# Kernel optimization log

Hardware: AMD Instinct MI355X
Metric: run time of the kernel (lower is better)

Reference implementation:

```python
import jax, jax.numpy as jnp
import numpy as np


def setup_inputs() -> dict:
    key = jax.random.key(0)
    k1, k2, k3, k4 = jax.random.split(key, 4)
    bs, n, f_in, f_out, n_head = 4, 2048, 64, 64, 8
    h = jax.random.normal(k1, (bs, n, f_in), dtype=jnp.float32)
    adj = jnp.ones((bs, n, n), dtype=bool)  # accepted by forward but unused
    # xavier-uniform-like init scales
    w = jax.random.uniform(k2, (n_head, f_in, f_out), dtype=jnp.float32,
                           minval=-1.0, maxval=1.0) * np.sqrt(6.0 / (f_in + f_out))
    a_src = jax.random.uniform(k3, (n_head, f_out, 1), dtype=jnp.float32,
                               minval=-1.0, maxval=1.0) * np.sqrt(6.0 / (f_out + 1))
    a_dst = jax.random.uniform(k4, (n_head, f_out, 1), dtype=jnp.float32,
                               minval=-1.0, maxval=1.0) * np.sqrt(6.0 / (f_out + 1))
    bias_p = jnp.zeros((f_out,), dtype=jnp.float32)
    return {"h": h, "adj": adj, "w": w, "a_src": a_src, "a_dst": a_dst, "bias_p": bias_p}


def reference(h, adj, w, a_src, a_dst, bias_p):
    # h: [b, n, f_in], w: [h, f_in, f_out]
    h_prime = jnp.einsum('bnf,hfo->bhno', h, w)          # [b, h, n, f_out]
    t = jnp.tanh(h_prime)
    attn_src = jnp.einsum('bhno,ho->bhn', t, a_src[..., 0])  # [b, h, n]
    attn_dst = jnp.einsum('bhno,ho->bhn', t, a_dst[..., 0])  # [b, h, n]
    # attn[b,h,i,j] = src[b,h,i] + dst[b,h,j]  (dense; adj unused in original)
    attn = attn_src[..., :, None] + attn_dst[..., None, :]   # [b, h, n, n]
    attn = jnp.where(attn >= 0, attn, 0.2 * attn)            # leaky_relu(0.2)
    attn = jax.nn.softmax(attn, axis=-1)
    # dropout p=0.0 -> identity
    out = jnp.einsum('bhij,bhjo->bhio', attn, h_prime)       # [b, h, n, f_out]
    return out + bias_p
```

## Files before the change

kernel.cpp:

```cpp
#include <hip/hip_runtime.h>
#include <hip/hip_bf16.h>

#define NN 2048
#define FF 64
#define NH 8
#define BDIM 4
#define BH 32

typedef __attribute__((ext_vector_type(8))) short short8;
typedef __attribute__((ext_vector_type(4))) float floatx4;
typedef __attribute__((ext_vector_type(4))) unsigned uint4v;

__device__ __forceinline__ float LDIN(const void* p, size_t i, int b16) {
    return b16 ? __bfloat162float(((const __hip_bfloat16*)p)[i]) : ((const float*)p)[i];
}
__device__ __forceinline__ unsigned packhi(float f0, float f1) {
    return __builtin_amdgcn_perm(__float_as_uint(f1), __float_as_uint(f0), 0x07060302);
}
__device__ __forceinline__ float hitrunc(float x) {
    return __uint_as_float(__float_as_uint(x) & 0xFFFF0000u);
}
__device__ __forceinline__ ushort bf16bits(float v) {
    __hip_bfloat16 b = __float2bfloat16(v);
    return __builtin_bit_cast(ushort, b);
}
__device__ __forceinline__ int SWZ(int row, int col) {
    return row * 64 + ((((col >> 3) ^ (row & 7)) << 3) | (col & 7));
}
__device__ __forceinline__ float fast_tanh(float v) {
    float ex = __expf(2.0f * v);
    return 1.0f - 2.0f * __builtin_amdgcn_rcpf(ex + 1.0f);
}

__global__ __launch_bounds__(256) void k_proj(
    const void* __restrict__ h, const void* __restrict__ w,
    const void* __restrict__ asrc, const void* __restrict__ adst,
    ushort* __restrict__ hpTt, float* __restrict__ rArr,
    float* __restrict__ edHa, float* __restrict__ edLa, int* __restrict__ flagOut)
{
    const int t  = threadIdx.x;
    const int rt = blockIdx.x & 31;
    const int hd = (blockIdx.x >> 5) & 7;
    const int b  = blockIdx.x >> 8;
    const int bh = b * NH + hd;
    const int r0 = rt * 64;

    __shared__ int sb16;
    __shared__ ushort SH[4 * 64 * 64];
    ushort* bHi = SH;
    ushort* bLo = SH + 64 * 64;
    ushort* aHi = SH + 2 * 64 * 64;
    ushort* aLo = SH + 3 * 64 * 64;

    if (t < 64) {
        unsigned word = ((const unsigned*)h)[t];
        unsigned lowexp = (word >> 7) & 0xFFu;
        bool plaus = (lowexp >= 96u && lowexp <= 159u);
        unsigned long long m = __ballot(plaus);
        if (t == 0) sb16 = (__popcll(m) >= 48) ? 1 : 0;
    }
    __syncthreads();
    const int b16 = sb16;
    if (blockIdx.x == 0 && t == 0) flagOut[0] = b16;

    const int lane = t & 63, wv = t >> 6;
    const int ml = lane & 15, q = lane >> 4;

    if (b16) {
        const ushort* wp = (const ushort*)w + (size_t)hd * FF * FF;
        const int n = t & 63, kq4 = (t >> 6) * 4;
#pragma unroll
        for (int g = 0; g < 4; ++g) {
            int kb = g * 16 + kq4;
            ushort v0 = wp[(kb + 0) * FF + n];
            ushort v1 = wp[(kb + 1) * FF + n];
            ushort v2 = wp[(kb + 2) * FF + n];
            ushort v3 = wp[(kb + 3) * FF + n];
            uint2 pk = { (unsigned)v0 | ((unsigned)v1 << 16),
                         (unsigned)v2 | ((unsigned)v3 << 16) };
            *(uint2*)&bHi[SWZ(n, kb)] = pk;
        }
        const ushort* hsrc = (const ushort*)h + (size_t)(b * NN + r0) * FF;
        for (int g = t; g < 512; g += 256) {
            int row = g >> 3, c8 = (g & 7) * 8;
            uint4v u = *(const uint4v*)(hsrc + row * FF + c8);
            *(uint4v*)&aHi[SWZ(row, c8)] = u;
        }
    } else {
        const float* wp = (const float*)w + (size_t)hd * FF * FF;
        const int n = t & 63, kq4 = (t >> 6) * 4;
#pragma unroll
        for (int g = 0; g < 4; ++g) {
            int kb = g * 16 + kq4;
            float x0 = wp[(kb + 0) * FF + n];
            float x1 = wp[(kb + 1) * FF + n];
            float x2 = wp[(kb + 2) * FF + n];
            float x3 = wp[(kb + 3) * FF + n];
            uint2 hi2 = { packhi(x0, x1), packhi(x2, x3) };
            uint2 lo2 = { packhi(x0 - hitrunc(x0), x1 - hitrunc(x1)),
                          packhi(x2 - hitrunc(x2), x3 - hitrunc(x3)) };
            *(uint2*)&bHi[SWZ(n, kb)] = hi2;
            *(uint2*)&bLo[SWZ(n, kb)] = lo2;
        }
        const float* hsrc = (const float*)h + (size_t)(b * NN + r0) * FF;
        for (int g = t; g < 1024; g += 256) {
            int row = g >> 4, c4 = (g & 15) * 4;
            floatx4 x = *(const floatx4*)(hsrc + row * FF + c4);
            uint2 hi2 = { packhi(x[0], x[1]), packhi(x[2], x[3]) };
            uint2 lo2 = { packhi(x[0] - hitrunc(x[0]), x[1] - hitrunc(x[1])),
                          packhi(x[2] - hitrunc(x[2]), x[3] - hitrunc(x[3])) };
            *(uint2*)&aHi[SWZ(row, c4)] = hi2;
            *(uint2*)&aLo[SWZ(row, c4)] = lo2;
        }
    }
    __syncthreads();

    short8 ah[2], al[2];
#pragma unroll
    for (int kc = 0; kc < 2; ++kc) {
        ah[kc] = *(const short8*)&aHi[SWZ(wv * 16 + ml, kc * 32 + q * 8)];
        if (!b16) al[kc] = *(const short8*)&aLo[SWZ(wv * 16 + ml, kc * 32 + q * 8)];
    }
    short8 bhf[4][2], blf[4][2];
#pragma unroll
    for (int nt = 0; nt < 4; ++nt)
#pragma unroll
        for (int kc = 0; kc < 2; ++kc) {
            bhf[nt][kc] = *(const short8*)&bHi[SWZ(nt * 16 + ml, kc * 32 + q * 8)];
            if (!b16) blf[nt][kc] = *(const short8*)&bLo[SWZ(nt * 16 + ml, kc * 32 + q * 8)];
        }

    float aS[4], aD[4];
#pragma unroll
    for (int nt = 0; nt < 4; ++nt) {
        aS[nt] = LDIN(asrc, hd * FF + nt * 16 + ml, b16);
        aD[nt] = LDIN(adst, hd * FF + nt * 16 + ml, b16);
    }

    floatx4 acc[4];
#pragma unroll
    for (int nt = 0; nt < 4; ++nt) {
        floatx4 a = {0.f, 0.f, 0.f, 0.f};
        if (b16) {
#pragma unroll
            for (int kc = 0; kc < 2; ++kc)
                a = __builtin_amdgcn_mfma_f32_16x16x32_bf16(ah[kc], bhf[nt][kc], a, 0, 0, 0);
        } else {
#pragma unroll
            for (int kc = 0; kc < 2; ++kc) {
                a = __builtin_amdgcn_mfma_f32_16x16x32_bf16(ah[kc], bhf[nt][kc], a, 0, 0, 0);
                a = __builtin_amdgcn_mfma_f32_16x16x32_bf16(ah[kc], blf[nt][kc], a, 0, 0, 0);
                a = __builtin_amdgcn_mfma_f32_16x16x32_bf16(al[kc], bhf[nt][kc], a, 0, 0, 0);
            }
        }
        acc[nt] = a;
    }

    __syncthreads();
    ushort* trans = SH;
#pragma unroll
    for (int nt = 0; nt < 4; ++nt) {
        ushort b0 = bf16bits(acc[nt][0]), b1 = bf16bits(acc[nt][1]);
        ushort b2 = bf16bits(acc[nt][2]), b3 = bf16bits(acc[nt][3]);
        uint2 pk = { (unsigned)b0 | ((unsigned)b1 << 16),
                     (unsigned)b2 | ((unsigned)b3 << 16) };
        *(uint2*)&trans[SWZ(nt * 16 + ml, wv * 16 + q * 4)] = pk;
    }

    float ps[4] = {0.f, 0.f, 0.f, 0.f}, pd[4] = {0.f, 0.f, 0.f, 0.f};
#pragma unroll
    for (int nt = 0; nt < 4; ++nt)
#pragma unroll
        for (int reg = 0; reg < 4; ++reg) {
            float tv = fast_tanh(acc[nt][reg]);
            ps[reg] += tv * aS[nt];
            pd[reg] += tv * aD[nt];
        }
#pragma unroll
    for (int msk = 1; msk < 16; msk <<= 1)
#pragma unroll
        for (int reg = 0; reg < 4; ++reg) {
            ps[reg] += __shfl_xor(ps[reg], msk, 64);
            pd[reg] += __shfl_xor(pd[reg], msk, 64);
        }
    if (ml == 0) {
#pragma unroll
        for (int reg = 0; reg < 4; ++reg) {
            int i = bh * NN + r0 + wv * 16 + q * 4 + reg;
            float sv = ps[reg], dv = pd[reg];
            rArr[i] = __expf(-0.8f * sv);
            edHa[i] = __expf(dv);
            edLa[i] = __expf(0.2f * dv);
        }
    }
    __syncthreads();
    {
        const int o = t >> 2, part = (t & 3) * 16;
        uint4v v0 = *(const uint4v*)&trans[SWZ(o, part)];
        uint4v v1 = *(const uint4v*)&trans[SWZ(o, part + 8)];
        ushort* dst = hpTt + (((size_t)bh * 32 + rt) * 64 + o) * 64 + part;
        *(uint4v*)dst = v0;
        *(uint4v*)(dst + 8) = v1;
    }
}

__global__ __launch_bounds__(512) void k_attn(
    const ushort* __restrict__ hpTt, const float* __restrict__ rArr,
    const float* __restrict__ edHa, const float* __restrict__ edLa,
    const void* __restrict__ bias, const int* __restrict__ flag,
    void* __restrict__ out)
{
    const int b16 = flag[0];
    const int t = threadIdx.x;
    const int wv = t >> 6, lane = t & 63;
    const int ml = lane & 15, q = lane >> 4;
    const int bh = blockIdx.x & 31;
    const int i0 = (blockIdx.x >> 5) * 128 + wv * 16;

    __shared__ ushort Bc[2][64 * 64];
    __shared__ __align__(16) float ehS[NN];
    __shared__ __align__(16) float elS[NN];

    ((floatx4*)ehS)[t] = ((const floatx4*)(edHa + bh * NN))[t];
    ((floatx4*)elS)[t] = ((const floatx4*)(edLa + bh * NN))[t];

    const ushort* src = hpTt + (size_t)bh * NN * FF;
    const float r = rArr[bh * NN + i0 + ml];

    const short8 ONESB = {0x3F80, 0x3F80, 0x3F80, 0x3F80,
                          0x3F80, 0x3F80, 0x3F80, 0x3F80};

    floatx4 acc[4];
#pragma unroll
    for (int nt = 0; nt < 4; ++nt) acc[nt] = (floatx4){0.f, 0.f, 0.f, 0.f};
    floatx4 accD = {0.f, 0.f, 0.f, 0.f};

    auto stage = [&](int c, int buf) {
        uint4v u = *(const uint4v*)(src + (size_t)c * 4096 + t * 8);
        *(uint4v*)&Bc[buf][SWZ(t >> 3, (t & 7) * 8)] = u;
    };

    auto compute = [&](int c, int buf) {
        const int j0 = c * 64;
#pragma unroll
        for (int ks = 0; ks < 2; ++ks) {
            const int col = ks * 32 + q * 8;
            floatx4 eh0 = *(const floatx4*)&ehS[j0 + col];
            floatx4 eh1 = *(const floatx4*)&ehS[j0 + col + 4];
            floatx4 el0 = *(const floatx4*)&elS[j0 + col];
            floatx4 el1 = *(const floatx4*)&elS[j0 + col + 4];
            short8 Bf[4];
#pragma unroll
            for (int nt = 0; nt < 4; ++nt)
                Bf[nt] = *(const short8*)&Bc[buf][SWZ(nt * 16 + ml, col)];
            float p[8];
#pragma unroll
            for (int j = 0; j < 4; ++j) {
                p[j]     = fmaxf(eh0[j], r * el0[j]);
                p[j + 4] = fmaxf(eh1[j], r * el1[j]);
            }
            uint4v hv = { packhi(p[0], p[1]), packhi(p[2], p[3]),
                          packhi(p[4], p[5]), packhi(p[6], p[7]) };
            short8 PH = __builtin_bit_cast(short8, hv);
#pragma unroll
            for (int nt = 0; nt < 4; ++nt)
                acc[nt] = __builtin_amdgcn_mfma_f32_16x16x32_bf16(PH, Bf[nt], acc[nt], 0, 0, 0);
            accD = __builtin_amdgcn_mfma_f32_16x16x32_bf16(PH, ONESB, accD, 0, 0, 0);
        }
    };

    stage(0, 0);
    __syncthreads();
    for (int c = 0; c < 32; ++c) {
        const int buf = c & 1;
        if (c < 31) stage(c + 1, buf ^ 1);
        compute(c, buf);
        __syncthreads();
    }

    float biasv[4];
#pragma unroll
    for (int nt = 0; nt < 4; ++nt) biasv[nt] = LDIN(bias, nt * 16 + ml, b16);

#pragma unroll
    for (int reg = 0; reg < 4; ++reg) {
        float inv = 1.0f / accD[reg];
        int i = i0 + q * 4 + reg;
#pragma unroll
        for (int nt = 0; nt < 4; ++nt) {
            float val = acc[nt][reg] * inv + biasv[nt];
            size_t oi = ((size_t)bh * NN + i) * FF + nt * 16 + ml;
            if (b16) ((__hip_bfloat16*)out)[oi] = __float2bfloat16(val);
            else     ((float*)out)[oi] = val;
        }
    }
}

extern "C" void kernel_launch(void* const* d_in, const int* in_sizes, int n_in,
                              void* d_out, int out_size, void* d_ws, size_t ws_size,
                              hipStream_t stream) {
    const void* h    = d_in[0];
    const void* w    = d_in[2];
    const void* asrc = d_in[3];
    const void* adst = d_in[4];
    const void* bias = d_in[5];

    float* ws = (float*)d_ws;
    int*    flag = (int*)ws;
    ushort* hpTt = (ushort*)(ws + 16);
    float*  rArr = (float*)(hpTt + (size_t)BH * NN * FF);
    float*  edHa = rArr + BH * NN;
    float*  edLa = edHa + BH * NN;

    k_proj<<<BDIM * NH * 32, 256, 0, stream>>>(h, w, asrc, adst,
                                               hpTt, rArr, edHa, edLa, flag);
    k_attn<<<BH * 16, 512, 0, stream>>>(hpTt, rArr, edHa, edLa,
                                        bias, flag, d_out);
}
```

Measured before the change: 139.8 us.

## Pre-split weights into MFMA fragment layout and double chunk staging in attention

A new k_prep kernel converts each head's weight matrix once into hi/lo bf16 fragments in MFMA-ready order. k_proj then loads those fragments straight from global memory instead of re-gathering and splitting weights in every block through shared memory, which also drops one barrier and reduces LDS use. k_attn moves from a 2-deep to a 4-slot buffer, staging two 64-row chunks per iteration so it needs half as many barriers. The cost is an extra kernel launch and twice the LDS for the attention tiles, which may lower occupancy.

Result: no change. 138.7 us (-0.7%).

```diff
diff --git a/kernel.cpp b/kernel.cpp
--- a/kernel.cpp
+++ b/kernel.cpp
@@ -31,12 +31,63 @@
     float ex = __expf(2.0f * v);
     return 1.0f - 2.0f * __builtin_amdgcn_rcpf(ex + 1.0f);
 }
+__device__ __forceinline__ int sniff_b16(const void* h) {
+    unsigned word = ((const unsigned*)h)[threadIdx.x & 63];
+    unsigned lowexp = (word >> 7) & 0xFFu;
+    bool plaus = (lowexp >= 96u && lowexp <= 159u);
+    unsigned long long m = __ballot(plaus);
+    return (__popcll(m) >= 48) ? 1 : 0;
+}
+
+__global__ __launch_bounds__(256) void k_prep(
+    const void* __restrict__ h, const void* __restrict__ w,
+    ushort* __restrict__ wF, int* __restrict__ flagOut)
+{
+    const int hd = blockIdx.x, t = threadIdx.x;
+    __shared__ int sb16;
+    if (t < 64) {
+        int f = sniff_b16(h);
+        if (t == 0) { sb16 = f; if (hd == 0) flagOut[0] = f; }
+    }
+    __syncthreads();
+    const int b16 = sb16;
+
+#pragma unroll
+    for (int g = 0; g < 2; ++g) {
+        int gi = t * 2 + g;
+        int ml = gi & 15, q = (gi >> 4) & 3, kc = (gi >> 6) & 1, nt = (gi >> 7) & 3;
+        int n = nt * 16 + ml, kb = kc * 32 + q * 8;
+        size_t off = (size_t)hd * 4096 + ((nt * 2 + kc) * 4 + q) * 128 + ml * 8;
+        if (b16) {
+            const ushort* wp = (const ushort*)w + (size_t)hd * FF * FF;
+            ushort hi[8];
+#pragma unroll
+            for (int j = 0; j < 8; ++j) hi[j] = wp[(kb + j) * FF + n];
+            *(uint4v*)&wF[off] = __builtin_bit_cast(uint4v, *(short8*)hi);
+            short8 z = {0, 0, 0, 0, 0, 0, 0, 0};
+            *(uint4v*)&wF[off + 32768] = __builtin_bit_cast(uint4v, z);
+        } else {
+            const float* wp = (const float*)w + (size_t)hd * FF * FF;
+            float x[8];
+#pragma unroll
+            for (int j = 0; j < 8; ++j) x[j] = wp[(kb + j) * FF + n];
+            uint4v hv = { packhi(x[0], x[1]), packhi(x[2], x[3]),
+                          packhi(x[4], x[5]), packhi(x[6], x[7]) };
+            uint4v lv = { packhi(x[0] - hitrunc(x[0]), x[1] - hitrunc(x[1])),
+                          packhi(x[2] - hitrunc(x[2]), x[3] - hitrunc(x[3])),
+                          packhi(x[4] - hitrunc(x[4]), x[5] - hitrunc(x[5])),
+                          packhi(x[6] - hitrunc(x[6]), x[7] - hitrunc(x[7])) };
+            *(uint4v*)&wF[off] = hv;
+            *(uint4v*)&wF[off + 32768] = lv;
+        }
+    }
+}
 
 __global__ __launch_bounds__(256) void k_proj(
-    const void* __restrict__ h, const void* __restrict__ w,
+    const void* __restrict__ h, const ushort* __restrict__ wF,
     const void* __restrict__ asrc, const void* __restrict__ adst,
     ushort* __restrict__ hpTt, float* __restrict__ rArr,
-    float* __restrict__ edHa, float* __restrict__ edLa, int* __restrict__ flagOut)
+    float* __restrict__ edHa, float* __restrict__ edLa)
 {
     const int t  = threadIdx.x;
     const int rt = blockIdx.x & 31;
@@ -46,64 +97,33 @@
     const int r0 = rt * 64;
 
     __shared__ int sb16;
-    __shared__ ushort SH[4 * 64 * 64];
-    ushort* bHi = SH;
-    ushort* bLo = SH + 64 * 64;
-    ushort* aHi = SH + 2 * 64 * 64;
-    ushort* aLo = SH + 3 * 64 * 64;
-
+    __shared__ ushort aHi[64 * 64];
+    __shared__ ushort aLo[64 * 64];
+    __shared__ ushort trans[64 * 64];
     if (t < 64) {
-        unsigned word = ((const unsigned*)h)[t];
-        unsigned lowexp = (word >> 7) & 0xFFu;
-        bool plaus = (lowexp >= 96u && lowexp <= 159u);
-        unsigned long long m = __ballot(plaus);
-        if (t == 0) sb16 = (__popcll(m) >= 48) ? 1 : 0;
+        int f = sniff_b16(h);
+        if (t == 0) sb16 = f;
     }
     __syncthreads();
     const int b16 = sb16;
-    if (blockIdx.x == 0 && t == 0) flagOut[0] = b16;
 
     const int lane = t & 63, wv = t >> 6;
     const int ml = lane & 15, q = lane >> 4;
 
     if (b16) {
-        const ushort* wp = (const ushort*)w + (size_t)hd * FF * FF;
-        const int n = t & 63, kq4 = (t >> 6) * 4;
-#pragma unroll
-        for (int g = 0; g < 4; ++g) {
-            int kb = g * 16 + kq4;
-            ushort v0 = wp[(kb + 0) * FF + n];
-            ushort v1 = wp[(kb + 1) * FF + n];
-            ushort v2 = wp[(kb + 2) * FF + n];
-            ushort v3 = wp[(kb + 3) * FF + n];
-            uint2 pk = { (unsigned)v0 | ((unsigned)v1 << 16),
-                         (unsigned)v2 | ((unsigned)v3 << 16) };
-            *(uint2*)&bHi[SWZ(n, kb)] = pk;
-        }
         const ushort* hsrc = (const ushort*)h + (size_t)(b * NN + r0) * FF;
-        for (int g = t; g < 512; g += 256) {
+#pragma unroll
+        for (int g0 = 0; g0 < 2; ++g0) {
+            int g = t + g0 * 256;
             int row = g >> 3, c8 = (g & 7) * 8;
             uint4v u = *(const uint4v*)(hsrc + row * FF + c8);
             *(uint4v*)&aHi[SWZ(row, c8)] = u;
         }
     } else {
-        const float* wp = (const float*)w + (size_t)hd * FF * FF;
-        const int n = t & 63, kq4 = (t >> 6) * 4;
-#pragma unroll
-        for (int g = 0; g < 4; ++g) {
-            int kb = g * 16 + kq4;
-            float x0 = wp[(kb + 0) * FF + n];
-            float x1 = wp[(kb + 1) * FF + n];
-            float x2 = wp[(kb + 2) * FF + n];
-            float x3 = wp[(kb + 3) * FF + n];
-            uint2 hi2 = { packhi(x0, x1), packhi(x2, x3) };
-            uint2 lo2 = { packhi(x0 - hitrunc(x0), x1 - hitrunc(x1)),
-                          packhi(x2 - hitrunc(x2), x3 - hitrunc(x3)) };
-            *(uint2*)&bHi[SWZ(n, kb)] = hi2;
-            *(uint2*)&bLo[SWZ(n, kb)] = lo2;
-        }
         const float* hsrc = (const float*)h + (size_t)(b * NN + r0) * FF;
-        for (int g = t; g < 1024; g += 256) {
+#pragma unroll
+        for (int g0 = 0; g0 < 4; ++g0) {
+            int g = t + g0 * 256;
             int row = g >> 4, c4 = (g & 15) * 4;
             floatx4 x = *(const floatx4*)(hsrc + row * FF + c4);
             uint2 hi2 = { packhi(x[0], x[1]), packhi(x[2], x[3]) };
@@ -122,12 +142,14 @@
         if (!b16) al[kc] = *(const short8*)&aLo[SWZ(wv * 16 + ml, kc * 32 + q * 8)];
     }
     short8 bhf[4][2], blf[4][2];
+    const ushort* wfh = wF + (size_t)hd * 4096;
 #pragma unroll
     for (int nt = 0; nt < 4; ++nt)
 #pragma unroll
         for (int kc = 0; kc < 2; ++kc) {
-            bhf[nt][kc] = *(const short8*)&bHi[SWZ(nt * 16 + ml, kc * 32 + q * 8)];
-            if (!b16) blf[nt][kc] = *(const short8*)&bLo[SWZ(nt * 16 + ml, kc * 32 + q * 8)];
+            size_t off = ((nt * 2 + kc) * 4 + q) * 128 + ml * 8;
+            bhf[nt][kc] = __builtin_bit_cast(short8, *(const uint4v*)&wfh[off]);
+            if (!b16) blf[nt][kc] = __builtin_bit_cast(short8, *(const uint4v*)&wfh[off + 32768]);
         }
 
     float aS[4], aD[4];
@@ -156,8 +178,6 @@
         acc[nt] = a;
     }
 
-    __syncthreads();
-    ushort* trans = SH;
 #pragma unroll
     for (int nt = 0; nt < 4; ++nt) {
         ushort b0 = bf16bits(acc[nt][0]), b1 = bf16bits(acc[nt][1]);
@@ -217,7 +237,7 @@
     const int bh = blockIdx.x & 31;
     const int i0 = (blockIdx.x >> 5) * 128 + wv * 16;
 
-    __shared__ ushort Bc[2][64 * 64];
+    __shared__ ushort Bc[4][64 * 64];
     __shared__ __align__(16) float ehS[NN];
     __shared__ __align__(16) float elS[NN];
 
@@ -235,13 +255,13 @@
     for (int nt = 0; nt < 4; ++nt) acc[nt] = (floatx4){0.f, 0.f, 0.f, 0.f};
     floatx4 accD = {0.f, 0.f, 0.f, 0.f};
 
-    auto stage = [&](int c, int buf) {
+    auto stage = [&](int c) {
         uint4v u = *(const uint4v*)(src + (size_t)c * 4096 + t * 8);
-        *(uint4v*)&Bc[buf][SWZ(t >> 3, (t & 7) * 8)] = u;
+        *(uint4v*)&Bc[c & 3][SWZ(t >> 3, (t & 7) * 8)] = u;
     };
 
-    auto compute = [&](int c, int buf) {
-        const int j0 = c * 64;
+    auto compute = [&](int c) {
+        const int j0 = c * 64, buf = c & 3;
 #pragma unroll
         for (int ks = 0; ks < 2; ++ks) {
             const int col = ks * 32 + q * 8;
@@ -269,12 +289,12 @@
         }
     };
 
-    stage(0, 0);
-    __syncthreads();
-    for (int c = 0; c < 32; ++c) {
-        const int buf = c & 1;
-        if (c < 31) stage(c + 1, buf ^ 1);
-        compute(c, buf);
+    stage(0); stage(1);
+    __syncthreads();
+    for (int c = 0; c < 32; c += 2) {
+        if (c + 2 < 32) { stage(c + 2); stage(c + 3); }
+        compute(c);
+        compute(c + 1);
         __syncthreads();
     }
 
@@ -311,9 +331,11 @@
     float*  rArr = (float*)(hpTt + (size_t)BH * NN * FF);
     float*  edHa = rArr + BH * NN;
     float*  edLa = edHa + BH * NN;
-
-    k_proj<<<BDIM * NH * 32, 256, 0, stream>>>(h, w, asrc, adst,
-                                               hpTt, rArr, edHa, edLa, flag);
+    ushort* wF   = (ushort*)(edLa + BH * NN);
+
+    k_prep<<<NH, 256, 0, stream>>>(h, w, wF, flag);
+    k_proj<<<BDIM * NH * 32, 256, 0, stream>>>(h, wF, asrc, adst,
+                                               hpTt, rArr, edHa, edLa);
     k_attn<<<BH * 16, 512, 0, stream>>>(hpTt, rArr, edHa, edLa,
                                         bias, flag, d_out);
 }
```
